# Kernel tuning notes

Measured on AMD Instinct MI355X. Metric: run time of the kernel, lower is better.

Reference implementation:

```python
import jax, jax.numpy as jnp
import numpy as np

N_NODES = 50000


def _glorot(key, fan_in, fan_out):
    lim = jnp.sqrt(6.0 / (fan_in + fan_out)).astype(jnp.float32)
    return jax.random.uniform(key, (fan_in, fan_out), jnp.float32, -lim, lim)


def gcn_layer(x, W, b, src, dst, deg_inv_sqrt):
    # PyG GCNConv: x' = D^{-1/2} (A + I) D^{-1/2} (x W) + b
    h = x @ W  # [N, F_out]
    norm = deg_inv_sqrt[src] * deg_inv_sqrt[dst]  # [E+N]
    msg = norm[:, None] * h[src]                  # gather + scale
    out = jax.ops.segment_sum(msg, dst, num_segments=x.shape[0])
    return out + b


def setup_inputs() -> dict:
    key = jax.random.key(0)
    ks = jax.random.split(key, 8)
    in_c, out_c = 128, 64
    hid = 2 * out_c
    x = jax.random.normal(ks[0], (N_NODES, in_c), jnp.float32)
    edge_index = jax.random.randint(ks[1], (2, 800000), 0, N_NODES, jnp.int64)
    return {
        "x": x,
        "edge_index": edge_index,
        "W1": _glorot(ks[2], in_c, hid), "b1": jnp.zeros((hid,), jnp.float32),
        "W2": _glorot(ks[3], hid, hid),  "b2": jnp.zeros((hid,), jnp.float32),
        "W3": _glorot(ks[4], hid, out_c), "b3": jnp.zeros((out_c,), jnp.float32),
    }


def reference(x, edge_index, W1, b1, W2, b2, W3, b3):
    n = x.shape[0]
    loops = jnp.arange(n, dtype=edge_index.dtype)
    src = jnp.concatenate([edge_index[0], loops])  # [E+N]
    dst = jnp.concatenate([edge_index[1], loops])
    deg = jax.ops.segment_sum(jnp.ones_like(dst, dtype=x.dtype), dst, num_segments=n)
    deg_inv_sqrt = jnp.where(deg > 0, jax.lax.rsqrt(deg), 0.0)

    h = jax.nn.relu(gcn_layer(x, W1, b1, src, dst, deg_inv_sqrt))
    h = jax.nn.relu(gcn_layer(h, W2, b2, src, dst, deg_inv_sqrt))
    return gcn_layer(h, W3, b3, src, dst, deg_inv_sqrt)
```

## Files before the change

kernel.cpp:

```cpp
#include <hip/hip_runtime.h>
#include <hip/hip_bf16.h>
#include <hip/hip_fp16.h>
#include <cstdint>
#include <cstddef>

typedef _Float16 half8_t __attribute__((ext_vector_type(8)));
typedef float f32x4 __attribute__((ext_vector_type(4)));


__global__ __launch_bounds__(256) void zero_kernel(int* __restrict__ p, int n) {
  int i = (blockIdx.x * 256 + threadIdx.x) * 4;
  if (i + 4 <= n) {
    *(int4*)&p[i] = make_int4(0, 0, 0, 0);
  } else {
    for (; i < n; ++i) p[i] = 0;
  }
}


__global__ __launch_bounds__(256) void countpos_kernel(const int* __restrict__ dst,
                                                       int* __restrict__ cnt,
                                                       int* __restrict__ pos, int E) {
  int e = (blockIdx.x * blockDim.x + threadIdx.x) * 4;
  if (e + 4 <= E) {
    int4 d = *(const int4*)&dst[e];
    int p0 = atomicAdd(&cnt[d.x], 1);
    int p1 = atomicAdd(&cnt[d.y], 1);
    int p2 = atomicAdd(&cnt[d.z], 1);
    int p3 = atomicAdd(&cnt[d.w], 1);
    *(int4*)&pos[e] = make_int4(p0, p1, p2, p3);
  } else {
    for (; e < E; ++e) pos[e] = atomicAdd(&cnt[dst[e]], 1);
  }
}

__global__ __launch_bounds__(256) void place_kernel(const int* __restrict__ src,
                                                    const int* __restrict__ dst,
                                                    const int* __restrict__ pos,
                                                    const int* __restrict__ rp,
                                                    int* __restrict__ ss, int E) {
  int e = (blockIdx.x * blockDim.x + threadIdx.x) * 4;
  if (e + 4 <= E) {
    int4 d = *(const int4*)&dst[e];
    int4 p = *(const int4*)&pos[e];
    int4 s = *(const int4*)&src[e];
    int r0 = rp[d.x], r1 = rp[d.y], r2 = rp[d.z], r3 = rp[d.w];
    ss[r0 + p.x] = s.x;
    ss[r1 + p.y] = s.y;
    ss[r2 + p.z] = s.z;
    ss[r3 + p.w] = s.w;
  } else {
    for (; e < E; ++e) ss[rp[dst[e]] + pos[e]] = src[e];
  }
}

__global__ __launch_bounds__(256) void block_sum_kernel(const int* __restrict__ cnt,
                                                        int* __restrict__ bsum, int N) {
  const int tid = threadIdx.x, lane = tid & 63, wid = tid >> 6;
  __shared__ int wt[4];
  int base = blockIdx.x * 2048 + tid * 8;
  int s = 0;
#pragma unroll
  for (int q = 0; q < 8; ++q) { int i = base + q; if (i < N) s += cnt[i]; }
#pragma unroll
  for (int off = 32; off; off >>= 1) s += __shfl_down(s, off);
  if (lane == 0) wt[wid] = s;
  __syncthreads();
  if (tid == 0) bsum[blockIdx.x] = wt[0] + wt[1] + wt[2] + wt[3];
}

__global__ __launch_bounds__(256) void scan_bsum_kernel(const int* __restrict__ bsum,
                                                        int* __restrict__ boff,
                                                        int NB, int E, int* __restrict__ rpN) {
  __shared__ int sh[256];
  const int tid = threadIdx.x;
  int v = (tid < NB) ? bsum[tid] : 0;
  sh[tid] = v;
  __syncthreads();
  for (int off = 1; off < 256; off <<= 1) {
    int t = (tid >= off) ? sh[tid - off] : 0;
    __syncthreads();
    sh[tid] += t;
    __syncthreads();
  }
  if (tid < NB) boff[tid] = sh[tid] - v;
  if (tid == 0) rpN[0] = E;
}

__global__ __launch_bounds__(256) void scan_apply_kernel(const int* __restrict__ cnt,
                                                         const int* __restrict__ boff,
                                                         int* __restrict__ rp,
                                                         float* __restrict__ dis, int N) {
  const int tid = threadIdx.x, lane = tid & 63, wid = tid >> 6;
  __shared__ int wtot[4], wexc[4];
  int base = blockIdx.x * 2048 + tid * 8;
  int v[8]; int s = 0;
#pragma unroll
  for (int q = 0; q < 8; ++q) { int i = base + q; int x = (i < N) ? cnt[i] : 0; v[q] = x; s += x; }
  int sc = s;
#pragma unroll
  for (int off = 1; off < 64; off <<= 1) { int t = __shfl_up(sc, off); if (lane >= off) sc += t; }
  if (lane == 63) wtot[wid] = sc;
  __syncthreads();
  if (tid == 0) { int r = 0; for (int wq = 0; wq < 4; ++wq) { wexc[wq] = r; r += wtot[wq]; } }
  __syncthreads();
  int thr = boff[blockIdx.x] + wexc[wid] + (sc - s);
#pragma unroll
  for (int q = 0; q < 8; ++q) {
    int i = base + q;
    if (i < N) { rp[i] = thr; dis[i] = rsqrtf((float)(v[q] + 1)); }
    thr += v[q];
  }
}


__global__ __launch_bounds__(256) void cvt_x_kernel(const float* __restrict__ X,
                                                    _Float16* __restrict__ Xh, int total) {
  int i = (blockIdx.x * 256 + threadIdx.x) * 8;
  if (i + 8 <= total) {
    float4 a = *(const float4*)&X[i];
    float4 b = *(const float4*)&X[i + 4];
    half8_t o;
    o[0] = (_Float16)a.x; o[1] = (_Float16)a.y; o[2] = (_Float16)a.z; o[3] = (_Float16)a.w;
    o[4] = (_Float16)b.x; o[5] = (_Float16)b.y; o[6] = (_Float16)b.z; o[7] = (_Float16)b.w;
    *(half8_t*)&Xh[i] = o;
  } else {
    for (; i < total; ++i) Xh[i] = (_Float16)X[i];
  }
}

__global__ __launch_bounds__(256) void cvt_wT_kernel(const float* __restrict__ W,
                                                     _Float16* __restrict__ Wt, int K, int C) {
  int i = blockIdx.x * 256 + threadIdx.x;
  if (i < K * C) {
    int k = i / C, c = i % C;
    Wt[(size_t)c * K + k] = (_Float16)W[i];
  }
}


template <int COUT, int WM, int WN>
__global__ __launch_bounds__(256) void mfma_gemm_kernel(const half8_t* __restrict__ Xh,
                                                        const half8_t* __restrict__ Wt,
                                                        const float* __restrict__ dis,
                                                        _Float16* __restrict__ G, int N) {
  const int wave = threadIdx.x >> 6;
  const int lane = threadIdx.x & 63;
  const int wm = wave / WN, wn = wave % WN;
  const int row0 = blockIdx.x * (WM * 64) + wm * 64;
  const int col0 = wn * 64;
  const int lr = lane & 15;
  const int lk = lane >> 4;
  f32x4 acc[4][4];
#pragma unroll
  for (int r = 0; r < 4; ++r)
#pragma unroll
    for (int c = 0; c < 4; ++c) acc[r][c] = (f32x4){0.f, 0.f, 0.f, 0.f};

#pragma unroll
  for (int ks = 0; ks < 4; ++ks) {
    half8_t a[4], b[4];
#pragma unroll
    for (int r = 0; r < 4; ++r) {
      int row = row0 + r * 16 + lr;
      half8_t az = {};
      a[r] = (row < N) ? Xh[(size_t)row * 16 + ks * 4 + lk] : az;
    }
#pragma unroll
    for (int c = 0; c < 4; ++c) {
      int col = col0 + c * 16 + lr;
      b[c] = Wt[(size_t)col * 16 + ks * 4 + lk];
    }
#pragma unroll
    for (int r = 0; r < 4; ++r)
#pragma unroll
      for (int c = 0; c < 4; ++c)
        acc[r][c] = __builtin_amdgcn_mfma_f32_16x16x32_f16(a[r], b[c], acc[r][c], 0, 0, 0);
  }

#pragma unroll
  for (int r = 0; r < 4; ++r) {
#pragma unroll
    for (int q = 0; q < 4; ++q) {
      int row = row0 + r * 16 + lk * 4 + q;
      if (row < N) {
        float dv = dis[row];
#pragma unroll
        for (int c = 0; c < 4; ++c) {
          G[(size_t)row * COUT + col0 + c * 16 + lr] = (_Float16)(acc[r][c][q] * dv);
        }
      }
    }
  }
}


template <bool RELU>
__global__ __launch_bounds__(256) void agg128_kernel(const _Float16* __restrict__ G,
                                                     const int* __restrict__ rp,
                                                     const int* __restrict__ ss,
                                                     const float* __restrict__ dis,
                                                     const float* __restrict__ bias,
                                                     _Float16* __restrict__ H, int N) {
  const int wave = threadIdx.x >> 6;
  const int lane = threadIdx.x & 63;
  const int grp = lane >> 4;
  const int sub = lane & 15;
  const int w = blockIdx.x * 16 + wave * 4 + grp;
  if (w >= N) return;
  const int e0 = rp[w], e1 = rp[w + 1];
  float acc[8];
  half8_t sv = *(const half8_t*)&G[(size_t)w * 128 + sub * 8];
#pragma unroll
  for (int j = 0; j < 8; ++j) acc[j] = (float)sv[j];
  int e = e0;
  for (; e + 8 <= e1; e += 8) {
    int jj[8];
#pragma unroll
    for (int q = 0; q < 8; ++q) jj[q] = ss[e + q];
    half8_t v[8];
#pragma unroll
    for (int q = 0; q < 8; ++q) v[q] = *(const half8_t*)&G[(size_t)jj[q] * 128 + sub * 8];
#pragma unroll
    for (int j = 0; j < 8; ++j)
      acc[j] += (((float)v[0][j] + (float)v[1][j]) + ((float)v[2][j] + (float)v[3][j])) +
                (((float)v[4][j] + (float)v[5][j]) + ((float)v[6][j] + (float)v[7][j]));
  }
  for (; e + 2 <= e1; e += 2) {
    int i0 = ss[e], i1 = ss[e + 1];
    half8_t v0 = *(const half8_t*)&G[(size_t)i0 * 128 + sub * 8];
    half8_t v1 = *(const half8_t*)&G[(size_t)i1 * 128 + sub * 8];
#pragma unroll
    for (int j = 0; j < 8; ++j) acc[j] += (float)v0[j] + (float)v1[j];
  }
  for (; e < e1; ++e) {
    half8_t v0 = *(const half8_t*)&G[(size_t)ss[e] * 128 + sub * 8];
#pragma unroll
    for (int j = 0; j < 8; ++j) acc[j] += (float)v0[j];
  }
  float d = dis[w];
  float4 b0 = *(const float4*)&bias[sub * 8];
  float4 b1 = *(const float4*)&bias[sub * 8 + 4];
  float bb[8] = {b0.x, b0.y, b0.z, b0.w, b1.x, b1.y, b1.z, b1.w};
  half8_t o;
#pragma unroll
  for (int j = 0; j < 8; ++j) {
    float v = d * acc[j] + bb[j];
    if (RELU) v = fmaxf(v, 0.f);
    o[j] = (_Float16)v;
  }
  *(half8_t*)&H[(size_t)w * 128 + sub * 8] = o;
}

__global__ __launch_bounds__(256) void agg64_kernel(const _Float16* __restrict__ G,
                                                    const int* __restrict__ rp,
                                                    const int* __restrict__ ss,
                                                    const float* __restrict__ dis,
                                                    const float* __restrict__ bias,
                                                    float* __restrict__ OUT, int N) {
  const int wave = threadIdx.x >> 6;
  const int lane = threadIdx.x & 63;
  const int grp = lane >> 3;
  const int sub = lane & 7;
  const int w = blockIdx.x * 32 + wave * 8 + grp;
  if (w >= N) return;
  const int e0 = rp[w], e1 = rp[w + 1];
  float acc[8];
  half8_t sv = *(const half8_t*)&G[(size_t)w * 64 + sub * 8];
#pragma unroll
  for (int j = 0; j < 8; ++j) acc[j] = (float)sv[j];
  int e = e0;
  for (; e + 8 <= e1; e += 8) {
    int jj[8];
#pragma unroll
    for (int q = 0; q < 8; ++q) jj[q] = ss[e + q];
    half8_t v[8];
#pragma unroll
    for (int q = 0; q < 8; ++q) v[q] = *(const half8_t*)&G[(size_t)jj[q] * 64 + sub * 8];
#pragma unroll
    for (int j = 0; j < 8; ++j)
      acc[j] += (((float)v[0][j] + (float)v[1][j]) + ((float)v[2][j] + (float)v[3][j])) +
                (((float)v[4][j] + (float)v[5][j]) + ((float)v[6][j] + (float)v[7][j]));
  }
  for (; e + 2 <= e1; e += 2) {
    int i0 = ss[e], i1 = ss[e + 1];
    half8_t v0 = *(const half8_t*)&G[(size_t)i0 * 64 + sub * 8];
    half8_t v1 = *(const half8_t*)&G[(size_t)i1 * 64 + sub * 8];
#pragma unroll
    for (int j = 0; j < 8; ++j) acc[j] += (float)v0[j] + (float)v1[j];
  }
  for (; e < e1; ++e) {
    half8_t v0 = *(const half8_t*)&G[(size_t)ss[e] * 64 + sub * 8];
#pragma unroll
    for (int j = 0; j < 8; ++j) acc[j] += (float)v0[j];
  }
  float d = dis[w];
  float4 b0 = *(const float4*)&bias[sub * 8];
  float4 b1 = *(const float4*)&bias[sub * 8 + 4];
  float4 o0, o1;
  o0.x = d * acc[0] + b0.x; o0.y = d * acc[1] + b0.y;
  o0.z = d * acc[2] + b0.z; o0.w = d * acc[3] + b0.w;
  o1.x = d * acc[4] + b1.x; o1.y = d * acc[5] + b1.y;
  o1.z = d * acc[6] + b1.z; o1.w = d * acc[7] + b1.w;
  *(float4*)&OUT[(size_t)w * 64 + sub * 8] = o0;
  *(float4*)&OUT[(size_t)w * 64 + sub * 8 + 4] = o1;
}


extern "C" void kernel_launch(void* const* d_in, const int* in_sizes, int n_in,
                              void* d_out, int out_size, void* d_ws, size_t ws_size,
                              hipStream_t stream) {
  const float* x  = (const float*)d_in[0];
  const int*   ei = (const int*)d_in[1];
  const float* W1 = (const float*)d_in[2];
  const float* b1 = (const float*)d_in[3];
  const float* W2 = (const float*)d_in[4];
  const float* b2 = (const float*)d_in[5];
  const float* W3 = (const float*)d_in[6];
  const float* b3 = (const float*)d_in[7];

  const int inC = in_sizes[2] / in_sizes[3];
  const int N = in_sizes[0] / inC;
  const int E = in_sizes[1] / 2;

  auto align256 = [](size_t v) { return (v + 255) & ~(size_t)255; };
  char* p = (char*)d_ws;
  int* cnt = (int*)p;   p += align256((size_t)N * 4);
  int* rp  = (int*)p;   p += align256((size_t)(N + 1) * 4);
  int* ss  = (int*)p;   p += align256((size_t)E * 4);
  int* pos = (int*)p;   p += align256((size_t)E * 4);
  float* dis = (float*)p; p += align256((size_t)N * 4);
  _Float16* xh = (_Float16*)p; p += align256((size_t)N * 128 * 2);
  _Float16* g  = (_Float16*)p; p += align256((size_t)N * 128 * 2);
  _Float16* hh = (_Float16*)p; p += align256((size_t)N * 128 * 2);
  _Float16* wt1 = (_Float16*)p; p += align256((size_t)128 * 128 * 2);
  _Float16* wt2 = (_Float16*)p; p += align256((size_t)128 * 128 * 2);
  _Float16* wt3 = (_Float16*)p; p += align256((size_t)128 * 64 * 2);
  int* bsum = (int*)p;  p += align256(1024 * 4);
  int* boff = (int*)p;  p += align256(1024 * 4);

  const int* srcv = ei;
  const int* dstv = ei + E;

  const int NB = (N + 2047) / 2048;
  const int eB4 = (E / 4 + 255) / 256;

  zero_kernel<<<(N / 4 + 255) / 256, 256, 0, stream>>>(cnt, N);
  countpos_kernel<<<eB4, 256, 0, stream>>>(dstv, cnt, pos, E);
  block_sum_kernel<<<NB, 256, 0, stream>>>(cnt, bsum, N);
  scan_bsum_kernel<<<1, 256, 0, stream>>>(bsum, boff, NB, E, rp + N);
  scan_apply_kernel<<<NB, 256, 0, stream>>>(cnt, boff, rp, dis, N);
  place_kernel<<<eB4, 256, 0, stream>>>(srcv, dstv, pos, rp, ss, E);

  cvt_x_kernel<<<(N * 128 / 8 + 255) / 256, 256, 0, stream>>>(x, xh, N * 128);
  cvt_wT_kernel<<<(128 * 128 + 255) / 256, 256, 0, stream>>>(W1, wt1, 128, 128);
  cvt_wT_kernel<<<(128 * 128 + 255) / 256, 256, 0, stream>>>(W2, wt2, 128, 128);
  cvt_wT_kernel<<<(128 * 64 + 255) / 256, 256, 0, stream>>>(W3, wt3, 128, 64);

  const int g128B = (N + 127) / 128;
  const int g64B  = (N + 255) / 256;
  const int a128B = (N + 15) / 16;
  const int a64B  = (N + 31) / 32;

  mfma_gemm_kernel<128, 2, 2><<<g128B, 256, 0, stream>>>((const half8_t*)xh, (const half8_t*)wt1, dis, g, N);
  agg128_kernel<true><<<a128B, 256, 0, stream>>>(g, rp, ss, dis, b1, hh, N);
  mfma_gemm_kernel<128, 2, 2><<<g128B, 256, 0, stream>>>((const half8_t*)hh, (const half8_t*)wt2, dis, g, N);
  agg128_kernel<true><<<a128B, 256, 0, stream>>>(g, rp, ss, dis, b2, hh, N);
  mfma_gemm_kernel<64, 4, 1><<<g64B, 256, 0, stream>>>((const half8_t*)hh, (const half8_t*)wt3, dis, g, N);
  agg64_kernel<<<a64B, 256, 0, stream>>>(g, rp, ss, dis, b3, (float*)d_out, N);
}
```

Before: 203.8 us.

## Fuse aggregation with next-layer GEMM and fold input/weight conversions into prep kernels

The layer-1 and layer-2 aggregation kernels now also compute the next layer's GEMM. Each block aggregates 64 nodes into shared memory, then runs MFMA on them, so the intermediate H buffer never travels through global memory. The first GEMM converts fp32 X to fp16 on the fly instead of running a separate conversion pass. Zeroing and the three weight transposes are merged into one prep kernel, which cuts the launch count. In exchange, each aggregation block is larger and serialised across 4 iterations, and the block needs shared memory, which can lower occupancy and latency hiding for the gather-bound phase.

```diff
diff --git a/kernel.cpp b/kernel.cpp
--- a/kernel.cpp
+++ b/kernel.cpp
@@ -8,12 +8,31 @@
 typedef float f32x4 __attribute__((ext_vector_type(4)));
 
 
-__global__ __launch_bounds__(256) void zero_kernel(int* __restrict__ p, int n) {
-  int i = (blockIdx.x * 256 + threadIdx.x) * 4;
-  if (i + 4 <= n) {
-    *(int4*)&p[i] = make_int4(0, 0, 0, 0);
-  } else {
-    for (; i < n; ++i) p[i] = 0;
+__global__ __launch_bounds__(256) void prep_kernel(int* __restrict__ cnt, int N4,
+                                                   const float* __restrict__ W1, _Float16* __restrict__ wt1,
+                                                   const float* __restrict__ W2, _Float16* __restrict__ wt2,
+                                                   const float* __restrict__ W3, _Float16* __restrict__ wt3) {
+  int i = blockIdx.x * 256 + threadIdx.x;
+  if (i < N4) {
+    *(int4*)&cnt[i * 4] = make_int4(0, 0, 0, 0);
+    return;
+  }
+  int j = i - N4;
+  if (j < 16384) {
+    int k = j >> 7, c = j & 127;
+    wt1[c * 128 + k] = (_Float16)W1[j];
+    return;
+  }
+  j -= 16384;
+  if (j < 16384) {
+    int k = j >> 7, c = j & 127;
+    wt2[c * 128 + k] = (_Float16)W2[j];
+    return;
+  }
+  j -= 16384;
+  if (j < 8192) {
+    int k = j >> 6, c = j & 63;
+    wt3[c * 128 + k] = (_Float16)W3[j];
   }
 }
 
@@ -114,40 +133,14 @@
 }
 
 
-__global__ __launch_bounds__(256) void cvt_x_kernel(const float* __restrict__ X,
-                                                    _Float16* __restrict__ Xh, int total) {
-  int i = (blockIdx.x * 256 + threadIdx.x) * 8;
-  if (i + 8 <= total) {
-    float4 a = *(const float4*)&X[i];
-    float4 b = *(const float4*)&X[i + 4];
-    half8_t o;
-    o[0] = (_Float16)a.x; o[1] = (_Float16)a.y; o[2] = (_Float16)a.z; o[3] = (_Float16)a.w;
-    o[4] = (_Float16)b.x; o[5] = (_Float16)b.y; o[6] = (_Float16)b.z; o[7] = (_Float16)b.w;
-    *(half8_t*)&Xh[i] = o;
-  } else {
-    for (; i < total; ++i) Xh[i] = (_Float16)X[i];
-  }
-}
-
-__global__ __launch_bounds__(256) void cvt_wT_kernel(const float* __restrict__ W,
-                                                     _Float16* __restrict__ Wt, int K, int C) {
-  int i = blockIdx.x * 256 + threadIdx.x;
-  if (i < K * C) {
-    int k = i / C, c = i % C;
-    Wt[(size_t)c * K + k] = (_Float16)W[i];
-  }
-}
-
-
-template <int COUT, int WM, int WN>
-__global__ __launch_bounds__(256) void mfma_gemm_kernel(const half8_t* __restrict__ Xh,
-                                                        const half8_t* __restrict__ Wt,
-                                                        const float* __restrict__ dis,
-                                                        _Float16* __restrict__ G, int N) {
+__global__ __launch_bounds__(256) void gemm1_kernel(const float* __restrict__ X,
+                                                    const half8_t* __restrict__ Wt,
+                                                    const float* __restrict__ dis,
+                                                    _Float16* __restrict__ G, int N) {
   const int wave = threadIdx.x >> 6;
   const int lane = threadIdx.x & 63;
-  const int wm = wave / WN, wn = wave % WN;
-  const int row0 = blockIdx.x * (WM * 64) + wm * 64;
+  const int wm = wave >> 1, wn = wave & 1;
+  const int row0 = blockIdx.x * 128 + wm * 64;
   const int col0 = wn * 64;
   const int lr = lane & 15;
   const int lk = lane >> 4;
@@ -163,8 +156,15 @@
 #pragma unroll
     for (int r = 0; r < 4; ++r) {
       int row = row0 + r * 16 + lr;
-      half8_t az = {};
-      a[r] = (row < N) ? Xh[(size_t)row * 16 + ks * 4 + lk] : az;
+      half8_t av = {};
+      if (row < N) {
+        const float* xp = &X[(size_t)row * 128 + ks * 32 + lk * 8];
+        float4 xa = *(const float4*)xp;
+        float4 xb = *(const float4*)(xp + 4);
+        av[0] = (_Float16)xa.x; av[1] = (_Float16)xa.y; av[2] = (_Float16)xa.z; av[3] = (_Float16)xa.w;
+        av[4] = (_Float16)xb.x; av[5] = (_Float16)xb.y; av[6] = (_Float16)xb.z; av[7] = (_Float16)xb.w;
+      }
+      a[r] = av;
     }
 #pragma unroll
     for (int c = 0; c < 4; ++c) {
@@ -186,71 +186,122 @@
       if (row < N) {
         float dv = dis[row];
 #pragma unroll
-        for (int c = 0; c < 4; ++c) {
-          G[(size_t)row * COUT + col0 + c * 16 + lr] = (_Float16)(acc[r][c][q] * dv);
-        }
-      }
-    }
-  }
-}
-
-
-template <bool RELU>
-__global__ __launch_bounds__(256) void agg128_kernel(const _Float16* __restrict__ G,
-                                                     const int* __restrict__ rp,
-                                                     const int* __restrict__ ss,
-                                                     const float* __restrict__ dis,
-                                                     const float* __restrict__ bias,
-                                                     _Float16* __restrict__ H, int N) {
+        for (int c = 0; c < 4; ++c)
+          G[(size_t)row * 128 + col0 + c * 16 + lr] = (_Float16)(acc[r][c][q] * dv);
+      }
+    }
+  }
+}
+
+
+template <int COUT>
+__global__ __launch_bounds__(256) void fused_agg_gemm_kernel(const _Float16* __restrict__ G,
+                                                             const int* __restrict__ rp,
+                                                             const int* __restrict__ ss,
+                                                             const float* __restrict__ dis,
+                                                             const float* __restrict__ bias,
+                                                             const half8_t* __restrict__ Wt,
+                                                             _Float16* __restrict__ G2, int N) {
+  __shared__ _Float16 sh[64][136];
   const int wave = threadIdx.x >> 6;
   const int lane = threadIdx.x & 63;
   const int grp = lane >> 4;
   const int sub = lane & 15;
-  const int w = blockIdx.x * 16 + wave * 4 + grp;
-  if (w >= N) return;
-  const int e0 = rp[w], e1 = rp[w + 1];
-  float acc[8];
-  half8_t sv = *(const half8_t*)&G[(size_t)w * 128 + sub * 8];
-#pragma unroll
-  for (int j = 0; j < 8; ++j) acc[j] = (float)sv[j];
-  int e = e0;
-  for (; e + 8 <= e1; e += 8) {
-    int jj[8];
-#pragma unroll
-    for (int q = 0; q < 8; ++q) jj[q] = ss[e + q];
-    half8_t v[8];
-#pragma unroll
-    for (int q = 0; q < 8; ++q) v[q] = *(const half8_t*)&G[(size_t)jj[q] * 128 + sub * 8];
-#pragma unroll
-    for (int j = 0; j < 8; ++j)
-      acc[j] += (((float)v[0][j] + (float)v[1][j]) + ((float)v[2][j] + (float)v[3][j])) +
-                (((float)v[4][j] + (float)v[5][j]) + ((float)v[6][j] + (float)v[7][j]));
-  }
-  for (; e + 2 <= e1; e += 2) {
-    int i0 = ss[e], i1 = ss[e + 1];
-    half8_t v0 = *(const half8_t*)&G[(size_t)i0 * 128 + sub * 8];
-    half8_t v1 = *(const half8_t*)&G[(size_t)i1 * 128 + sub * 8];
-#pragma unroll
-    for (int j = 0; j < 8; ++j) acc[j] += (float)v0[j] + (float)v1[j];
-  }
-  for (; e < e1; ++e) {
-    half8_t v0 = *(const half8_t*)&G[(size_t)ss[e] * 128 + sub * 8];
-#pragma unroll
-    for (int j = 0; j < 8; ++j) acc[j] += (float)v0[j];
-  }
-  float d = dis[w];
-  float4 b0 = *(const float4*)&bias[sub * 8];
-  float4 b1 = *(const float4*)&bias[sub * 8 + 4];
-  float bb[8] = {b0.x, b0.y, b0.z, b0.w, b1.x, b1.y, b1.z, b1.w};
-  half8_t o;
-#pragma unroll
-  for (int j = 0; j < 8; ++j) {
-    float v = d * acc[j] + bb[j];
-    if (RELU) v = fmaxf(v, 0.f);
-    o[j] = (_Float16)v;
-  }
-  *(half8_t*)&H[(size_t)w * 128 + sub * 8] = o;
-}
+  const int nb0 = blockIdx.x * 64;
+
+#pragma unroll
+  for (int it = 0; it < 4; ++it) {
+    const int wl = wave * 16 + it * 4 + grp;
+    const int w = nb0 + wl;
+    if (w < N) {
+      const int e0 = rp[w], e1 = rp[w + 1];
+      float acc[8];
+      half8_t sv = *(const half8_t*)&G[(size_t)w * 128 + sub * 8];
+#pragma unroll
+      for (int j = 0; j < 8; ++j) acc[j] = (float)sv[j];
+      int e = e0;
+      for (; e + 8 <= e1; e += 8) {
+        int jj[8];
+#pragma unroll
+        for (int q = 0; q < 8; ++q) jj[q] = ss[e + q];
+        half8_t v[8];
+#pragma unroll
+        for (int q = 0; q < 8; ++q) v[q] = *(const half8_t*)&G[(size_t)jj[q] * 128 + sub * 8];
+#pragma unroll
+        for (int j = 0; j < 8; ++j)
+          acc[j] += (((float)v[0][j] + (float)v[1][j]) + ((float)v[2][j] + (float)v[3][j])) +
+                    (((float)v[4][j] + (float)v[5][j]) + ((float)v[6][j] + (float)v[7][j]));
+      }
+      for (; e + 2 <= e1; e += 2) {
+        int i0 = ss[e], i1 = ss[e + 1];
+        half8_t v0 = *(const half8_t*)&G[(size_t)i0 * 128 + sub * 8];
+        half8_t v1 = *(const half8_t*)&G[(size_t)i1 * 128 + sub * 8];
+#pragma unroll
+        for (int j = 0; j < 8; ++j) acc[j] += (float)v0[j] + (float)v1[j];
+      }
+      for (; e < e1; ++e) {
+        half8_t v0 = *(const half8_t*)&G[(size_t)ss[e] * 128 + sub * 8];
+#pragma unroll
+        for (int j = 0; j < 8; ++j) acc[j] += (float)v0[j];
+      }
+      float d = dis[w];
+      float4 b0 = *(const float4*)&bias[sub * 8];
+      float4 b1 = *(const float4*)&bias[sub * 8 + 4];
+      float bb[8] = {b0.x, b0.y, b0.z, b0.w, b1.x, b1.y, b1.z, b1.w};
+      half8_t o;
+#pragma unroll
+      for (int j = 0; j < 8; ++j) {
+        float v = fmaxf(d * acc[j] + bb[j], 0.f);
+        o[j] = (_Float16)v;
+      }
+      *(half8_t*)&sh[wl][sub * 8] = o;
+    }
+  }
+  __syncthreads();
+
+  const int lr = lane & 15;
+  const int lk = lane >> 4;
+  constexpr int NC = COUT / 64;
+  const int col0 = wave * (COUT / 4);
+  f32x4 acc2[4][NC];
+#pragma unroll
+  for (int r = 0; r < 4; ++r)
+#pragma unroll
+    for (int c = 0; c < NC; ++c) acc2[r][c] = (f32x4){0.f, 0.f, 0.f, 0.f};
+
+#pragma unroll
+  for (int ks = 0; ks < 4; ++ks) {
+    half8_t a[4], b[NC];
+#pragma unroll
+    for (int r = 0; r < 4; ++r)
+      a[r] = *(const half8_t*)&sh[r * 16 + lr][ks * 32 + lk * 8];
+#pragma unroll
+    for (int c = 0; c < NC; ++c) {
+      int col = col0 + c * 16 + lr;
+      b[c] = Wt[(size_t)col * 16 + ks * 4 + lk];
+    }
+#pragma unroll
+    for (int r = 0; r < 4; ++r)
+#pragma unroll
+      for (int c = 0; c < NC; ++c)
+        acc2[r][c] = __builtin_amdgcn_mfma_f32_16x16x32_f16(a[r], b[c], acc2[r][c], 0, 0, 0);
+  }
+
+#pragma unroll
+  for (int r = 0; r < 4; ++r) {
+#pragma unroll
+    for (int q = 0; q < 4; ++q) {
+      int row = nb0 + r * 16 + lk * 4 + q;
+      if (row < N) {
+        float dv = dis[row];
+#pragma unroll
+        for (int c = 0; c < NC; ++c)
+          G2[(size_t)row * COUT + col0 + c * 16 + lr] = (_Float16)(acc2[r][c][q] * dv);
+      }
+    }
+  }
+}
+
 
 __global__ __launch_bounds__(256) void agg64_kernel(const _Float16* __restrict__ G,
                                                     const int* __restrict__ rp,
@@ -330,12 +381,11 @@
   int* ss  = (int*)p;   p += align256((size_t)E * 4);
   int* pos = (int*)p;   p += align256((size_t)E * 4);
   float* dis = (float*)p; p += align256((size_t)N * 4);
-  _Float16* xh = (_Float16*)p; p += align256((size_t)N * 128 * 2);
-  _Float16* g  = (_Float16*)p; p += align256((size_t)N * 128 * 2);
-  _Float16* hh = (_Float16*)p; p += align256((size_t)N * 128 * 2);
+  _Float16* gA = (_Float16*)p; p += align256((size_t)N * 128 * 2);
+  _Float16* gB = (_Float16*)p; p += align256((size_t)N * 128 * 2);
   _Float16* wt1 = (_Float16*)p; p += align256((size_t)128 * 128 * 2);
   _Float16* wt2 = (_Float16*)p; p += align256((size_t)128 * 128 * 2);
-  _Float16* wt3 = (_Float16*)p; p += align256((size_t)128 * 64 * 2);
+  _Float16* wt3 = (_Float16*)p; p += align256((size_t)64 * 128 * 2);
   int* bsum = (int*)p;  p += align256(1024 * 4);
   int* boff = (int*)p;  p += align256(1024 * 4);
 
@@ -344,28 +394,22 @@
 
   const int NB = (N + 2047) / 2048;
   const int eB4 = (E / 4 + 255) / 256;
-
-  zero_kernel<<<(N / 4 + 255) / 256, 256, 0, stream>>>(cnt, N);
+  const int N4 = (N + 3) / 4;
+  const int prepTot = N4 + 16384 + 16384 + 8192;
+
+  prep_kernel<<<(prepTot + 255) / 256, 256, 0, stream>>>(cnt, N4, W1, wt1, W2, wt2, W3, wt3);
   countpos_kernel<<<eB4, 256, 0, stream>>>(dstv, cnt, pos, E);
   block_sum_kernel<<<NB, 256, 0, stream>>>(cnt, bsum, N);
   scan_bsum_kernel<<<1, 256, 0, stream>>>(bsum, boff, NB, E, rp + N);
   scan_apply_kernel<<<NB, 256, 0, stream>>>(cnt, boff, rp, dis, N);
   place_kernel<<<eB4, 256, 0, stream>>>(srcv, dstv, pos, rp, ss, E);
 
-  cvt_x_kernel<<<(N * 128 / 8 + 255) / 256, 256, 0, stream>>>(x, xh, N * 128);
-  cvt_wT_kernel<<<(128 * 128 + 255) / 256, 256, 0, stream>>>(W1, wt1, 128, 128);
-  cvt_wT_kernel<<<(128 * 128 + 255) / 256, 256, 0, stream>>>(W2, wt2, 128, 128);
-  cvt_wT_kernel<<<(128 * 64 + 255) / 256, 256, 0, stream>>>(W3, wt3, 128, 64);
-
-  const int g128B = (N + 127) / 128;
-  const int g64B  = (N + 255) / 256;
-  const int a128B = (N + 15) / 16;
-  const int a64B  = (N + 31) / 32;
-
-  mfma_gemm_kernel<128, 2, 2><<<g128B, 256, 0, stream>>>((const half8_t*)xh, (const half8_t*)wt1, dis, g, N);
-  agg128_kernel<true><<<a128B, 256, 0, stream>>>(g, rp, ss, dis, b1, hh, N);
-  mfma_gemm_kernel<128, 2, 2><<<g128B, 256, 0, stream>>>((const half8_t*)hh, (const half8_t*)wt2, dis, g, N);
-  agg128_kernel<true><<<a128B, 256, 0, stream>>>(g, rp, ss, dis, b2, hh, N);
-  mfma_gemm_kernel<64, 4, 1><<<g64B, 256, 0, stream>>>((const half8_t*)hh, (const half8_t*)wt3, dis, g, N);
-  agg64_kernel<<<a64B, 256, 0, stream>>>(g, rp, ss, dis, b3, (float*)d_out, N);
-}
+  const int g1B = (N + 127) / 128;
+  const int fB  = (N + 63) / 64;
+  const int a64B = (N + 31) / 32;
+
+  gemm1_kernel<<<g1B, 256, 0, stream>>>(x, (const half8_t*)wt1, dis, gA, N);
+  fused_agg_gemm_kernel<128><<<fB, 256, 0, stream>>>(gA, rp, ss, dis, b1, (const half8_t*)wt2, gB, N);
+  fused_agg_gemm_kernel<64><<<fB, 256, 0, stream>>>(gB, rp, ss, dis, b2, (const half8_t*)wt3, gA, N);
+  agg64_kernel<<<a64B, 256, 0, stream>>>(gA, rp, ss, dis, b3, (float*)d_out, N);
+}
```

Result: faster. 180.3 us (-11.5%).
